# Optimization experiments

Hardware: AMD Instinct MI355X
Metric: run time of the kernel (lower is better)

Reference implementation:

```python
import jax, jax.numpy as jnp
import numpy as np

H = 150  # hidden size
STEPS = 10


def setup_inputs() -> dict:
    key = jax.random.key(0)
    ks = jax.random.split(key, 5)
    inputx = jax.random.normal(ks[0], (16, 1, H), dtype=jnp.float32)
    W_ih = jax.random.normal(ks[1], (4 * H, H), dtype=jnp.float32) * (1.0 / np.sqrt(H))
    W_hh = jax.random.normal(ks[2], (4 * H, H), dtype=jnp.float32) * (1.0 / np.sqrt(H))
    b_ih = jax.random.normal(ks[3], (4 * H,), dtype=jnp.float32) * (1.0 / np.sqrt(H))
    b_hh = jax.random.normal(ks[4], (4 * H,), dtype=jnp.float32) * (1.0 / np.sqrt(H))
    return {"inputx": inputx, "W_ih": W_ih, "W_hh": W_hh, "b_ih": b_ih, "b_hh": b_hh, "x": 13}


def _lstm_forward(inputx, W_ih, W_hh, b_ih, b_hh, x):
    # xs: the 10 steps inputx[x-10], ..., inputx[x-1], each [1, H]
    xs = inputx[x - STEPS:x]
    h0 = jnp.zeros((1, H), dtype=inputx.dtype)
    c0 = jnp.zeros((1, H), dtype=inputx.dtype)

    def step(carry, xt):
        h, c = carry
        # PyTorch LSTMCell: gates in order (i, f, g, o)
        gates = xt @ W_ih.T + b_ih + h @ W_hh.T + b_hh  # [1, 4H]
        i_g, f_g, g_g, o_g = jnp.split(gates, 4, axis=-1)
        c_new = jax.nn.sigmoid(f_g) * c + jax.nn.sigmoid(i_g) * jnp.tanh(g_g)
        h_new = jax.nn.sigmoid(o_g) * jnp.tanh(c_new)
        return (h_new, c_new), None

    (h_t, _), _ = jax.lax.scan(step, (h0, c0), xs)
    return h_t  # [1, H]


def reference(inputx, W_ih, W_hh, b_ih, b_hh, x):
    return _lstm_forward(inputx, W_ih, W_hh, b_ih, b_hh, x)
```

## Files before the change

kernel.cpp:

```cpp
#include <hip/hip_runtime.h>
#include <hip/hip_fp16.h>
#include <math.h>

#define H 150
#define G 600
#define STEPS 10
#define NT 320
#define WPR 76
#define NPK (WPR * G)
#define NGXB 19
#define NPKB 109
#define NPREP (NGXB + NPKB)
#define GXW 16
#define MAGIC 0x13579BDFu

#define GXP_WORDS (G * GXW)
#define SLOT_OFF (GXP_WORDS + NPK)

typedef _Float16 half2v __attribute__((ext_vector_type(2)));

__device__ __forceinline__ float sigm(float x) {
    return __builtin_amdgcn_rcpf(1.0f + __expf(-x));
}
__device__ __forceinline__ float ftanh(float x) {
    return 1.0f - 2.0f * __builtin_amdgcn_rcpf(1.0f + __expf(2.0f * x));
}
__device__ __forceinline__ float dot2(float acc, unsigned w, unsigned h) {
#if __has_builtin(__builtin_amdgcn_fdot2)
    return __builtin_amdgcn_fdot2(__builtin_bit_cast(half2v, w),
                                  __builtin_bit_cast(half2v, h), acc, false);
#else
    half2v wv = __builtin_bit_cast(half2v, w);
    half2v hv = __builtin_bit_cast(half2v, h);
    return acc + (float)wv.x * (float)hv.x + (float)wv.y * (float)hv.y;
#endif
}
__device__ __forceinline__ unsigned short f2h(float x) {
    _Float16 h = (_Float16)x;
    return __builtin_bit_cast(unsigned short, h);
}

__device__ __forceinline__ void st_agent(unsigned* p, unsigned v) {
    __hip_atomic_store(p, v, __ATOMIC_RELAXED, __HIP_MEMORY_SCOPE_AGENT);
}
__device__ __forceinline__ void st_agent_f(float* p, float v) {
    __hip_atomic_store(p, v, __ATOMIC_RELAXED, __HIP_MEMORY_SCOPE_AGENT);
}
__device__ __forceinline__ unsigned ld_agent(const unsigned* p) {
    return __hip_atomic_load(p, __ATOMIC_RELAXED, __HIP_MEMORY_SCOPE_AGENT);
}

__global__ __launch_bounds__(NT) void lstm_all(
    const float* __restrict__ inputx, const float* __restrict__ W_ih,
    const float* __restrict__ W_hh, const float* __restrict__ b_ih,
    const float* __restrict__ b_hh, const int* __restrict__ xp,
    float* __restrict__ gxp, unsigned* __restrict__ Wp,
    unsigned* __restrict__ slots, float* __restrict__ out)
{
    const int t   = threadIdx.x;
    const int blk = blockIdx.x;

    if (blk > 0) {
        const int p = blk - 1;
        if (p < NGXB) {
            int gid = p * NT + t;
            if (gid < STEPS * G) {
                int g  = gid / STEPS;
                int st = gid - g * STEPS;
                const float* xrow = inputx + (xp[0] - STEPS + st) * H;
                const float* wrow = W_ih + g * H;
                float a0 = 0.f, a1 = 0.f;
                #pragma unroll
                for (int k = 0; k < H; k += 2) {
                    float2 wv = *reinterpret_cast<const float2*>(wrow + k);
                    float2 xv = *reinterpret_cast<const float2*>(xrow + k);
                    a0 += wv.x * xv.x;
                    a1 += wv.y * xv.y;
                }
                st_agent_f(&gxp[g * GXW + st], a0 + a1 + b_ih[g] + b_hh[g]);
            }
        } else {
            for (int i = (p - NGXB) * NT + t; i < NPK; i += NPKB * NT) {
                int jh = i / 2400;
                int r  = i - jh * 2400;
                int g  = r >> 2;
                int j  = 4 * jh + (r & 3);
                unsigned v = 0;
                if (j < 75) {
                    const float* row = W_hh + g * H + 2 * j;
                    v = ((unsigned)f2h(row[1]) << 16) | (unsigned)f2h(row[0]);
                }
                st_agent(&Wp[i], v);
            }
        }
        __syncthreads();
        if (t == 0) st_agent(&slots[p], MAGIC);
        return;
    }

    __shared__ __align__(16) unsigned short s_hh[2 * WPR];
    __shared__ float2 s_ex[H];

    const bool work = (t < 300);
    const int r0 = (t < 150) ? t : t + 150;
    const int r1 = r0 + 150;

    unsigned w[2 * WPR];
    float gx0[STEPS], gx1[STEPS];

    auto load_all = [&]() {
        if (work) {
            const uint4* W4 = reinterpret_cast<const uint4*>(Wp);
            #pragma unroll
            for (int jh = 0; jh < 19; ++jh) {
                uint4 v = W4[jh * 600 + r0];
                w[4 * jh] = v.x; w[4 * jh + 1] = v.y;
                w[4 * jh + 2] = v.z; w[4 * jh + 3] = v.w;
            }
            #pragma unroll
            for (int jh = 0; jh < 19; ++jh) {
                uint4 v = W4[jh * 600 + r1];
                w[WPR + 4 * jh] = v.x; w[WPR + 4 * jh + 1] = v.y;
                w[WPR + 4 * jh + 2] = v.z; w[WPR + 4 * jh + 3] = v.w;
            }
            const float* ra = gxp + r0 * GXW;
            const float* rb = gxp + r1 * GXW;
            float4 q0 = *reinterpret_cast<const float4*>(ra);
            float4 q1 = *reinterpret_cast<const float4*>(ra + 4);
            float2 q2 = *reinterpret_cast<const float2*>(ra + 8);
            gx0[0]=q0.x; gx0[1]=q0.y; gx0[2]=q0.z; gx0[3]=q0.w;
            gx0[4]=q1.x; gx0[5]=q1.y; gx0[6]=q1.z; gx0[7]=q1.w;
            gx0[8]=q2.x; gx0[9]=q2.y;
            float4 p0 = *reinterpret_cast<const float4*>(rb);
            float4 p1 = *reinterpret_cast<const float4*>(rb + 4);
            float2 p2 = *reinterpret_cast<const float2*>(rb + 8);
            gx1[0]=p0.x; gx1[1]=p0.y; gx1[2]=p0.z; gx1[3]=p0.w;
            gx1[4]=p1.x; gx1[5]=p1.y; gx1[6]=p1.z; gx1[7]=p1.w;
            gx1[8]=p2.x; gx1[9]=p2.y;
        }
    };

    load_all();
    if (t < 2 * WPR) s_hh[t] = 0;

    int ok = 1;
    if (t < NPREP) ok = (ld_agent(&slots[t]) == MAGIC) ? 1 : 0;
    if (__syncthreads_and(ok) == 0) {
        if (t < NPREP) {
            while (ld_agent(&slots[t]) != MAGIC) __builtin_amdgcn_s_sleep(2);
        }
        __syncthreads();
        __threadfence();
        load_all();
        __syncthreads();
    }

    float c = 0.f;
    float si = 0.f, sf = 0.f;

    #pragma unroll 1
    for (int st = 0; st < STEPS; ++st) {
        if (work) {
            float a0 = 0.f, a1 = 0.f, a2 = 0.f, a3 = 0.f;
            float b0 = 0.f, b1 = 0.f, b2 = 0.f, b3 = 0.f;
            #pragma unroll
            for (int cc = 0; cc < 19; ++cc) {
                float4 hv = *reinterpret_cast<const float4*>(
                    reinterpret_cast<const char*>(s_hh) + 16 * cc);
                unsigned h0 = __float_as_uint(hv.x);
                unsigned h1 = __float_as_uint(hv.y);
                unsigned h2 = __float_as_uint(hv.z);
                unsigned h3 = __float_as_uint(hv.w);
                a0 = dot2(a0, w[4 * cc],     h0);
                a1 = dot2(a1, w[4 * cc + 1], h1);
                a2 = dot2(a2, w[4 * cc + 2], h2);
                a3 = dot2(a3, w[4 * cc + 3], h3);
                b0 = dot2(b0, w[WPR + 4 * cc],     h0);
                b1 = dot2(b1, w[WPR + 4 * cc + 1], h1);
                b2 = dot2(b2, w[WPR + 4 * cc + 2], h2);
                b3 = dot2(b3, w[WPR + 4 * cc + 3], h3);
            }
            float d0 = gx0[st] + (a0 + a1) + (a2 + a3);
            float d1 = gx1[st] + (b0 + b1) + (b2 + b3);
            if (t < 150) {
                si = sigm(d0);
                sf = sigm(d1);
            } else {
                s_ex[t - 150] = make_float2(ftanh(d0), sigm(d1));
            }
        }
        __syncthreads();
        if (t < 150) {
            float2 ex = s_ex[t];
            c = sf * c + si * ex.x;
            float h = ex.y * ftanh(c);
            if (st == STEPS - 1) out[t] = h;
            else                 s_hh[t] = f2h(h);
        }
        if (st < STEPS - 1) __syncthreads();
    }
}

__global__ __launch_bounds__(640) void lstm_fused(
    const float* __restrict__ inputx, const float* __restrict__ W_ih,
    const float* __restrict__ W_hh, const float* __restrict__ b_ih,
    const float* __restrict__ b_hh, const int* __restrict__ xp,
    float* __restrict__ out)
{
    __shared__ float s_h[H];
    __shared__ float s_c[H];
    __shared__ float s_gate[G];
    __shared__ float s_x[STEPS * H];

    const int tid = threadIdx.x;
    if (tid < H) { s_h[tid] = 0.f; s_c[tid] = 0.f; }
    const int x0 = (xp[0] - STEPS) * H;
    for (int i = tid; i < STEPS * H; i += 640) s_x[i] = inputx[x0 + i];
    __syncthreads();

    for (int t = 0; t < STEPS; ++t) {
        if (tid < G) {
            const float* wi = W_ih + tid * H;
            const float* wh = W_hh + tid * H;
            float acc = b_ih[tid] + b_hh[tid];
            for (int k = 0; k < H; ++k)
                acc += wi[k] * s_x[t * H + k] + wh[k] * s_h[k];
            s_gate[tid] = acc;
        }
        __syncthreads();
        if (tid < H) {
            float ig = s_gate[tid], fg = s_gate[H + tid];
            float gg = s_gate[2 * H + tid], og = s_gate[3 * H + tid];
            float cn = sigm(fg) * s_c[tid] + sigm(ig) * ftanh(gg);
            s_c[tid] = cn;
            s_h[tid] = sigm(og) * ftanh(cn);
        }
        __syncthreads();
    }
    if (tid < H) out[tid] = s_h[tid];
}

extern "C" void kernel_launch(void* const* d_in, const int* in_sizes, int n_in,
                              void* d_out, int out_size, void* d_ws, size_t ws_size,
                              hipStream_t stream) {
    const float* inputx = (const float*)d_in[0];
    const float* W_ih   = (const float*)d_in[1];
    const float* W_hh   = (const float*)d_in[2];
    const float* b_ih   = (const float*)d_in[3];
    const float* b_hh   = (const float*)d_in[4];
    const int*   xp     = (const int*)d_in[5];
    float* out = (float*)d_out;

    const size_t need = (size_t)(SLOT_OFF + NPREP) * sizeof(unsigned);
    if (ws_size >= need) {
        float*    gxp   = (float*)d_ws;
        unsigned* Wp    = (unsigned*)d_ws + GXP_WORDS;
        unsigned* slots = (unsigned*)d_ws + SLOT_OFF;
        lstm_all<<<NPREP + 1, NT, 0, stream>>>(inputx, W_ih, W_hh, b_ih, b_hh,
                                               xp, gxp, Wp, slots, out);
    } else {
        lstm_fused<<<1, 640, 0, stream>>>(inputx, W_ih, W_hh, b_ih, b_hh, xp, out);
    }
}
```

Measured before the change: 17.96 us.

## Pair gate rows across adjacent lanes, exchange via shuffles, double-buffer hidden state

Reassigns gate rows so each even/odd lane pair holds all four gates (i,f / g,o) of one hidden unit, and exchanges activations with lane shuffles instead of shared memory. This removes one __syncthreads per step and the s_ex staging buffer, and the hidden vector is now double-buffered so only one barrier per step is needed. Step 0 skips the matvec because h0 is zero. The tanh of g is computed through a shared exp/rcp path with a sign trick.

```diff
diff --git a/kernel.cpp b/kernel.cpp
--- a/kernel.cpp
+++ b/kernel.cpp
@@ -98,18 +98,32 @@
         return;
     }
 
-    __shared__ __align__(16) unsigned short s_hh[2 * WPR];
-    __shared__ float2 s_ex[H];
+    __shared__ __align__(16) unsigned short s_hh[2][160];
 
     const bool work = (t < 300);
-    const int r0 = (t < 150) ? t : t + 150;
-    const int r1 = r0 + 150;
+    const bool odd  = (t & 1);
+    const int r0 = (t >> 1) + (odd ? 150 : 0);
+    const int r1 = r0 + 300;
 
     unsigned w[2 * WPR];
     float gx0[STEPS], gx1[STEPS];
 
     auto load_all = [&]() {
         if (work) {
+            const float* ra = gxp + r0 * GXW;
+            const float* rb = gxp + r1 * GXW;
+            float4 q0 = *reinterpret_cast<const float4*>(ra);
+            float4 q1 = *reinterpret_cast<const float4*>(ra + 4);
+            float2 q2 = *reinterpret_cast<const float2*>(ra + 8);
+            float4 p0 = *reinterpret_cast<const float4*>(rb);
+            float4 p1 = *reinterpret_cast<const float4*>(rb + 4);
+            float2 p2 = *reinterpret_cast<const float2*>(rb + 8);
+            gx0[0]=q0.x; gx0[1]=q0.y; gx0[2]=q0.z; gx0[3]=q0.w;
+            gx0[4]=q1.x; gx0[5]=q1.y; gx0[6]=q1.z; gx0[7]=q1.w;
+            gx0[8]=q2.x; gx0[9]=q2.y;
+            gx1[0]=p0.x; gx1[1]=p0.y; gx1[2]=p0.z; gx1[3]=p0.w;
+            gx1[4]=p1.x; gx1[5]=p1.y; gx1[6]=p1.z; gx1[7]=p1.w;
+            gx1[8]=p2.x; gx1[9]=p2.y;
             const uint4* W4 = reinterpret_cast<const uint4*>(Wp);
             #pragma unroll
             for (int jh = 0; jh < 19; ++jh) {
@@ -123,25 +137,14 @@
                 w[WPR + 4 * jh] = v.x; w[WPR + 4 * jh + 1] = v.y;
                 w[WPR + 4 * jh + 2] = v.z; w[WPR + 4 * jh + 3] = v.w;
             }
-            const float* ra = gxp + r0 * GXW;
-            const float* rb = gxp + r1 * GXW;
-            float4 q0 = *reinterpret_cast<const float4*>(ra);
-            float4 q1 = *reinterpret_cast<const float4*>(ra + 4);
-            float2 q2 = *reinterpret_cast<const float2*>(ra + 8);
-            gx0[0]=q0.x; gx0[1]=q0.y; gx0[2]=q0.z; gx0[3]=q0.w;
-            gx0[4]=q1.x; gx0[5]=q1.y; gx0[6]=q1.z; gx0[7]=q1.w;
-            gx0[8]=q2.x; gx0[9]=q2.y;
-            float4 p0 = *reinterpret_cast<const float4*>(rb);
-            float4 p1 = *reinterpret_cast<const float4*>(rb + 4);
-            float2 p2 = *reinterpret_cast<const float2*>(rb + 8);
-            gx1[0]=p0.x; gx1[1]=p0.y; gx1[2]=p0.z; gx1[3]=p0.w;
-            gx1[4]=p1.x; gx1[5]=p1.y; gx1[6]=p1.z; gx1[7]=p1.w;
-            gx1[8]=p2.x; gx1[9]=p2.y;
         }
     };
 
     load_all();
-    if (t < 2 * WPR) s_hh[t] = 0;
+    {
+        unsigned short* sh = &s_hh[0][0];
+        sh[t] = 0;
+    }
 
     int ok = 1;
     if (t < NPREP) ok = (ld_agent(&slots[t]) == MAGIC) ? 1 : 0;
@@ -156,17 +159,40 @@
     }
 
     float c = 0.f;
-    float si = 0.f, sf = 0.f;
+    const float sgn = odd ? -1.f : 2.f;
+
+    auto act = [&](float d0, float d1, int st) {
+        if (work) {
+            float vA = sigm(d0);
+            float e  = __expf(sgn * d1);
+            float r  = __builtin_amdgcn_rcpf(1.f + e);
+            float vB = odd ? r : fmaf(-2.f, r, 1.f);
+            float sf = __shfl_xor(vA, 1);
+            float cn = fmaf(sf, c, vA * vB);
+            float ftc = ftanh(cn);
+            float ftco = __shfl_xor(ftc, 1);
+            if (!odd) c = cn;
+            else {
+                float h = vB * ftco;
+                if (st == STEPS - 1) out[t >> 1] = h;
+                else                 s_hh[st & 1][t >> 1] = f2h(h);
+            }
+        }
+    };
+
+    act(gx0[0], gx1[0], 0);
+    __syncthreads();
 
     #pragma unroll 1
-    for (int st = 0; st < STEPS; ++st) {
+    for (int st = 1; st < STEPS; ++st) {
+        float d0 = 0.f, d1 = 0.f;
         if (work) {
+            const char* hb = reinterpret_cast<const char*>(s_hh[(st + 1) & 1]);
             float a0 = 0.f, a1 = 0.f, a2 = 0.f, a3 = 0.f;
             float b0 = 0.f, b1 = 0.f, b2 = 0.f, b3 = 0.f;
             #pragma unroll
             for (int cc = 0; cc < 19; ++cc) {
-                float4 hv = *reinterpret_cast<const float4*>(
-                    reinterpret_cast<const char*>(s_hh) + 16 * cc);
+                float4 hv = *reinterpret_cast<const float4*>(hb + 16 * cc);
                 unsigned h0 = __float_as_uint(hv.x);
                 unsigned h1 = __float_as_uint(hv.y);
                 unsigned h2 = __float_as_uint(hv.z);
@@ -180,23 +206,10 @@
                 b2 = dot2(b2, w[WPR + 4 * cc + 2], h2);
                 b3 = dot2(b3, w[WPR + 4 * cc + 3], h3);
             }
-            float d0 = gx0[st] + (a0 + a1) + (a2 + a3);
-            float d1 = gx1[st] + (b0 + b1) + (b2 + b3);
-            if (t < 150) {
-                si = sigm(d0);
-                sf = sigm(d1);
-            } else {
-                s_ex[t - 150] = make_float2(ftanh(d0), sigm(d1));
-            }
-        }
-        __syncthreads();
-        if (t < 150) {
-            float2 ex = s_ex[t];
-            c = sf * c + si * ex.x;
-            float h = ex.y * ftanh(c);
-            if (st == STEPS - 1) out[t] = h;
-            else                 s_hh[t] = f2h(h);
-        }
+            d0 = gx0[st] + (a0 + a1) + (a2 + a3);
+            d1 = gx1[st] + (b0 + b1) + (b2 + b3);
+        }
+        act(d0, d1, st);
         if (st < STEPS - 1) __syncthreads();
     }
 }
```

Result: no change. 17.73 us (-1.3%).
